# Kernel optimization log

Hardware: AMD Instinct MI355X
Metric: run time of the kernel (lower is better)

The kernel has to match this reference:

```python
import jax, jax.numpy as jnp
import numpy as np

NC = 19
CH16, CH32 = 1024, 2048
B, H, W = 4, 64, 64
EPS = 1e-5


def bn_relu(x, gamma, beta):
    # Train-mode BatchNorm (batch statistics, as in torch default) + ReLU.
    axes = (0,) + tuple(range(2, x.ndim))  # reduce over batch + spatial
    mean = jnp.mean(x, axes, keepdims=True)
    var = jnp.var(x, axes, keepdims=True)
    shp = (1, -1) + (1,) * (x.ndim - 2)
    return jax.nn.relu((x - mean) * jax.lax.rsqrt(var + EPS) * gamma.reshape(shp) + beta.reshape(shp))


def setup_inputs() -> dict:
    key = jax.random.key(0)
    ks = jax.random.split(key, 10)
    def p(k, shape, fan):
        return jax.random.normal(k, shape, jnp.float32) / np.float32(np.sqrt(fan))
    ones = lambda c: jnp.ones((c,), jnp.float32)
    zeros = lambda c: jnp.zeros((c,), jnp.float32)
    return {
        "x": jax.random.normal(ks[0], (B, CH32, H, W), jnp.float32),
        "low_level_feature": jax.random.normal(ks[1], (B, CH16, H, W), jnp.float32),
        "W_L": p(ks[2], (NC, CH16), CH16), "b_L": zeros(NC),
        "W_X": p(ks[3], (512, CH32, 3, 3), CH32 * 9), "g_X": ones(512), "be_X": zeros(512),
        "W_phi": p(ks[4], (256, 512), 512), "g_phi": ones(256), "be_phi": zeros(256),
        "W_psi": p(ks[5], (256, 512), 512), "g_psi": ones(256), "be_psi": zeros(256),
        "W_delta": p(ks[6], (256, 512), 512), "g_delta": ones(256), "be_delta": zeros(256),
        "W_rho": p(ks[7], (512, 256), 256), "g_rho": ones(512), "be_rho": zeros(512),
        "W_g": p(ks[8], (512, 1024), 1024), "g_g": ones(512), "be_g": zeros(512),
        "W_out": p(ks[9], (NC, 512), 512), "b_out": zeros(NC),
    }


def reference(x, low_level_feature, W_L, b_L, W_X, g_X, be_X,
              W_phi, g_phi, be_phi, W_psi, g_psi, be_psi,
              W_delta, g_delta, be_delta, W_rho, g_rho, be_rho,
              W_g, g_g, be_g, W_out, b_out):
    b, _, h, w = x.shape
    # X = conv2d(2048->512, 3x3) + BN + ReLU
    Xf = jax.lax.conv_general_dilated(x, W_X, (1, 1), 'SAME',
                                      dimension_numbers=('NCHW', 'OIHW', 'NCHW'))
    Xf = bn_relu(Xf, g_X, be_X)                          # [b,512,h,w]
    # L = 1x1 conv (with bias) -> soft object regions
    L = jnp.einsum('bchw,nc->bnhw', low_level_feature, W_L) + b_L[None, :, None, None]
    l_flat = L.reshape(b, L.shape[1], -1)                # [b,nc,N]
    M = jax.nn.softmax(l_flat, axis=-1)                  # softmax over N
    X_flat = Xf.reshape(b, 512, -1)                      # [b,512,N]
    # f_k = (M @ X_flat^T)^T : object region features [b,512,nc]
    f_k = jnp.einsum('bkn,bcn->bck', M, X_flat)
    # phi/psi/delta: 1x1 conv1d + BN + ReLU
    query = bn_relu(jnp.einsum('oc,bck->bok', W_phi, f_k), g_phi, be_phi)      # [b,256,nc]
    key_ = bn_relu(jnp.einsum('oc,bcn->bon', W_psi, X_flat), g_psi, be_psi)    # [b,256,N]
    logit = jnp.einsum('bqk,bqn->bkn', query, key_)      # [b,nc,N]
    attn = jax.nn.softmax(logit, axis=1)                 # softmax over nc (dim 1)
    delta = bn_relu(jnp.einsum('oc,bck->bok', W_delta, f_k), g_delta, be_delta)  # [b,256,nc]
    attn_sum = jnp.einsum('bqk,bkn->bqn', delta, attn)   # [b,256,N]
    X_obj = bn_relu(jnp.einsum('oq,bqn->bon', W_rho, attn_sum), g_rho, be_rho)
    X_obj = X_obj.reshape(b, 512, h, w)
    concat = jnp.concatenate([Xf, X_obj], axis=1)        # [b,1024,h,w]
    X_bar = bn_relu(jnp.einsum('oc,bchw->bohw', W_g, concat), g_g, be_g)
    out = jnp.einsum('nc,bchw->bnhw', W_out, X_bar) + b_out[None, :, None, None]
    return out
```

## Files before the change

### kernel.cpp

```cpp
#include <hip/hip_runtime.h>
#include <hip/hip_bf16.h>
#include <cstdint>
#include <cstddef>

#define EPSV 1e-5f

typedef float f32x4 __attribute__((ext_vector_type(4)));
typedef _Float16 f16x8 __attribute__((ext_vector_type(8)));
typedef unsigned short ushortx8 __attribute__((ext_vector_type(8)));

__device__ __forceinline__ unsigned short f2h(float f) {
  _Float16 h = (_Float16)f;
  return *reinterpret_cast<unsigned short*>(&h);
}

__device__ __forceinline__ void gload16(const void* g, void* l) {
  __builtin_amdgcn_global_load_lds(
      (const __attribute__((address_space(1))) void*)g,
      (__attribute__((address_space(3))) void*)l, 16, 0, 0);
}

__global__ __launch_bounds__(256) void ocr_cvt_x(const float* __restrict__ x,
                                                 unsigned short* __restrict__ xT) {
  __shared__ float tile[64][65];
  int icb = blockIdx.x, h = blockIdx.y, b = blockIdx.z, t = threadIdx.x;
  const float* xp = x + ((size_t)b * 2048 + icb * 64) * 4096 + h * 64;
  #pragma unroll
  for (int r = 0; r < 16; ++r) {
    int icl = r * 4 + (t >> 6), w = t & 63;
    tile[icl][w] = xp[(size_t)icl * 4096 + w];
  }
  __syncthreads();
  #pragma unroll
  for (int it = 0; it < 2; ++it) {
    int w = it * 32 + (t >> 3), cb = (t & 7) * 8;
    ushortx8 o;
    #pragma unroll
    for (int j = 0; j < 8; ++j) o[j] = f2h(tile[cb + j][w]);
    *(ushortx8*)&xT[(((size_t)b * 66 + h + 1) * 66 + (w + 1)) * 2048 + icb * 64 + cb] = o;
  }
}

__global__ __launch_bounds__(256) void ocr_cvt_w(const float* __restrict__ Wx,
                                                 unsigned short* __restrict__ WT) {
  int oc = blockIdx.x >> 3;
  int ic = (blockIdx.x & 7) * 256 + threadIdx.x;
  const float* wp = Wx + ((size_t)oc * 2048 + ic) * 9;
  float v[9];
  #pragma unroll
  for (int t = 0; t < 9; ++t) v[t] = wp[t];
  #pragma unroll
  for (int t = 0; t < 9; ++t)
    WT[((size_t)t * 512 + oc) * 2048 + ic] = f2h(v[t]);
}

__global__ __launch_bounds__(256) void ocr_cvt_h2(const float* __restrict__ inA,
                                                  unsigned short* __restrict__ outA,
                                                  const float* __restrict__ inB,
                                                  unsigned short* __restrict__ outB) {
  int i = blockIdx.x * 256 + threadIdx.x;
  if (i < 131072) outA[i] = f2h(inA[i]);
  if (i < 524288) outB[i] = f2h(inB[i]);
}

__global__ __launch_bounds__(1024, 4) void ocr_conv_mfma(const unsigned short* __restrict__ xT,
                                                         const unsigned short* __restrict__ WT,
                                                         float* __restrict__ Xf) {
  __shared__ __align__(16) char lds_raw[163840];
  float* red = (float*)lds_raw;

  const int t = threadIdx.x;
  const int wv = t >> 6, lane = t & 63;
  const int kg = lane >> 4, lc = lane & 15;
  const int ws = wv & 7, kh = wv >> 3;

  const int hg  = blockIdx.x & 7;
  const int b   = (blockIdx.x >> 3) & 3;
  const int oct = blockIdx.x >> 5;
  const int oc0 = oct * 64, h0 = hg * 8;

  const char* gp[5]; int lo[5];
  #pragma unroll
  for (int i = 0; i < 5; ++i) {
    int c = wv * 5 + i;
    lo[i] = c * 1024;
    if (c < 38) {
      int cell = c * 64 + lane; if (cell > 2375) cell = 2375;
      int r = cell / 66, col = cell - r * 66; if (col > 63) col = 63;
      int tap = r >> 2, kgs = r & 3;
      gp[i] = (const char*)WT + (size_t)(((tap * 512 + oc0 + col) * 2048) + kgs * 8) * 2;
    } else {
      int c2 = c - 38;
      int cell = c2 * 64 + lane; if (cell > 2639) cell = 2639;
      int r = cell / 66, col = cell - r * 66;
      int row = r >> 2, kgs = r & 3;
      gp[i] = (const char*)xT + (size_t)((((b * 66 + h0 + row) * 66 + col) * 2048) + kgs * 8) * 2;
    }
  }

  f32x4 acc[4][4] = {};

  #pragma unroll
  for (int i = 0; i < 5; ++i) gload16(gp[i], lds_raw + lo[i]);
  __syncthreads();

  int cur = 0;
  #pragma unroll 1
  for (int step = 0; step < 64; ++step) {
    if (step < 63) {
      unsigned adv = (unsigned)(step + 1) * 64u;
      int nxt = (cur ^ 1) * 81920;
      #pragma unroll
      for (int i = 0; i < 5; ++i) gload16(gp[i] + adv, lds_raw + nxt + lo[i]);
    }
    const short* As = (const short*)(lds_raw + cur * 81920);
    const short* Bs = (const short*)(lds_raw + cur * 81920 + 38912);
    #pragma unroll
    for (int j = 0; j < 5; ++j) {
      const int tap = kh * 4 + j;
      const int dh = tap / 3, dw = tap - dh * 3;
      f16x8 av[4];
      #pragma unroll
      for (int mi = 0; mi < 4; ++mi)
        av[mi] = *(const f16x8*)&As[((tap * 4 + kg) * 66 + mi * 16 + lc) * 8];
      const int row = ws + dh;
      const int nw0 = (tap == 4) ? (kh ? 2 : 0) : 0;
      const int nwN = (tap == 4) ? (nw0 + 2) : 4;
      #pragma unroll
      for (int nw = 0; nw < 4; ++nw) {
        if (nw >= nw0 && nw < nwN) {
          f16x8 bv = *(const f16x8*)&Bs[((row * 4 + kg) * 66 + nw * 16 + lc + dw) * 8];
          #pragma unroll
          for (int mi = 0; mi < 4; ++mi)
            acc[mi][nw] = __builtin_amdgcn_mfma_f32_16x16x32_f16(av[mi], bv, acc[mi][nw], 0, 0, 0);
        }
      }
    }
    __syncthreads();
    cur ^= 1;
  }

  if (kh == 1) {
    #pragma unroll
    for (int mi = 0; mi < 4; ++mi)
      #pragma unroll
      for (int nw = 0; nw < 4; ++nw)
        *(f32x4*)&red[(((ws * 16 + mi * 4 + nw) * 64) + lane) * 4] = acc[mi][nw];
  }
  __syncthreads();
  if (kh == 0) {
    const int h = h0 + ws;
    #pragma unroll
    for (int mi = 0; mi < 4; ++mi) {
      #pragma unroll
      for (int nw = 0; nw < 4; ++nw) {
        f32x4 other = *(const f32x4*)&red[(((ws * 16 + mi * 4 + nw) * 64) + lane) * 4];
        f32x4 s = acc[mi][nw] + other;
        #pragma unroll
        for (int r = 0; r < 4; ++r) {
          int oc = oc0 + mi * 16 + (lane >> 4) * 4 + r;
          int w = nw * 16 + lc;
          Xf[(((size_t)b * 512 + oc) * 64 + h) * 64 + w] = s[r];
        }
      }
    }
  }
}

template<int K, int OT, int NT, int NWM, int NWN, int LDB>
__global__ __launch_bounds__(256) void ocr_gemm_h(const unsigned short* __restrict__ Ah,
                                                  const unsigned short* __restrict__ Bh,
                                                  float* __restrict__ Cm, int O) {
  static_assert(NT == 128, "NT fixed");
  constexpr int MI = OT / NWM / 16;
  constexpr int NI = NT / NWN / 16;
  constexpr int SA = OT + 2, SB = NT + 2;
  constexpr int ACELL = 4 * OT / 256;
  constexpr int ABUF = 4 * SA * 8;
  constexpr int BBUF = 4 * SB * 8;
  constexpr int NS = K / 32;
  constexpr int LPW = ACELL + 2;
  __shared__ __align__(16) short As_s[2 * ABUF];
  __shared__ __align__(16) short Bs_s[2 * BBUF];

  const int t = threadIdx.x;
  const int wv = t >> 6, lane = t & 63;
  const int kg = lane >> 4, lc = lane & 15;
  const int wm = wv / NWN, wn = wv % NWN;

  const int n0 = blockIdx.x * NT, o0 = blockIdx.y * OT, b = blockIdx.z;

  const char* aBase[ACELL]; int aLds[ACELL];
  #pragma unroll
  for (int r = 0; r < ACELL; ++r) {
    int flat0 = r * 256 + (t & 448);
    int flat  = flat0 + lane;
    int kgs = flat / OT, ol = flat % OT;
    aBase[r] = (const char*)(Ah + ((size_t)(o0 + ol)) * K + kgs * 8);
    aLds[r] = ((flat0 / OT) * SA + (flat0 % OT)) * 16;
  }
  const char* bBase[2]; int bLds[2];
  #pragma unroll
  for (int r = 0; r < 2; ++r) {
    int flat0 = r * 256 + (t & 448);
    int flat  = flat0 + lane;
    int kgs = flat >> 7, nl = flat & 127;
    bBase[r] = (const char*)(Bh + ((size_t)b * 4096 + n0 + nl) * LDB + kgs * 8);
    bLds[r] = ((flat0 >> 7) * SB + (flat0 & 127)) * 16;
  }

  f32x4 acc[MI][NI] = {};
  #pragma unroll
  for (int r = 0; r < ACELL; ++r) gload16(aBase[r], (char*)As_s + aLds[r]);
  #pragma unroll
  for (int r = 0; r < 2; ++r) gload16(bBase[r], (char*)Bs_s + bLds[r]);
  asm volatile("s_waitcnt vmcnt(0)" ::: "memory");
  __builtin_amdgcn_s_barrier();

  int cur = 0;
  #pragma unroll 1
  for (int step = 0; step < NS; ++step) {
    if (step + 1 < NS) {
      unsigned adv = (unsigned)(step + 1) * 64u;
      int nA = (cur ^ 1) * ABUF * 2, nB = (cur ^ 1) * BBUF * 2;
      #pragma unroll
      for (int r = 0; r < ACELL; ++r) gload16(aBase[r] + adv, (char*)As_s + nA + aLds[r]);
      #pragma unroll
      for (int r = 0; r < 2; ++r) gload16(bBase[r] + adv, (char*)Bs_s + nB + bLds[r]);
      if constexpr (LPW == 3) asm volatile("s_waitcnt vmcnt(3)" ::: "memory");
      else                    asm volatile("s_waitcnt vmcnt(4)" ::: "memory");
    } else {
      asm volatile("s_waitcnt vmcnt(0)" ::: "memory");
    }
    __builtin_amdgcn_s_barrier();

    const short* As = As_s + cur * ABUF;
    const short* Bsc = Bs_s + cur * BBUF;
    f16x8 av[MI], bv[NI];
    #pragma unroll
    for (int mi = 0; mi < MI; ++mi)
      av[mi] = *(const f16x8*)&As[(kg * SA + wm * (MI * 16) + mi * 16 + lc) * 8];
    #pragma unroll
    for (int ni = 0; ni < NI; ++ni)
      bv[ni] = *(const f16x8*)&Bsc[(kg * SB + wn * (NI * 16) + ni * 16 + lc) * 8];
    __builtin_amdgcn_s_setprio(1);
    #pragma unroll
    for (int mi = 0; mi < MI; ++mi)
      #pragma unroll
      for (int ni = 0; ni < NI; ++ni)
        acc[mi][ni] = __builtin_amdgcn_mfma_f32_16x16x32_f16(av[mi], bv[ni], acc[mi][ni], 0, 0, 0);
    __builtin_amdgcn_s_setprio(0);
    asm volatile("s_waitcnt lgkmcnt(0)" ::: "memory");
    __builtin_amdgcn_sched_barrier(0);
    __builtin_amdgcn_s_barrier();
    cur ^= 1;
  }
  #pragma unroll
  for (int mi = 0; mi < MI; ++mi) {
    #pragma unroll
    for (int ni = 0; ni < NI; ++ni) {
      int n = n0 + wn * (NI * 16) + ni * 16 + lc;
      #pragma unroll
      for (int r = 0; r < 4; ++r) {
        int oc = o0 + wm * (MI * 16) + mi * 16 + (lane >> 4) * 4 + r;
        Cm[((size_t)b * O + oc) * 4096 + n] = acc[mi][ni][r];
      }
    }
  }
}

__global__ __launch_bounds__(256) void ocr_t2h(const float* __restrict__ in,
                                               const float* __restrict__ scale,
                                               const float* __restrict__ shift,
                                               unsigned short* __restrict__ out,
                                               int C, int coff) {
  __shared__ float tile[64][65];
  int n0 = blockIdx.x * 64, c0 = blockIdx.y * 64, b = blockIdx.z;
  int t = threadIdx.x;
  #pragma unroll
  for (int r = 0; r < 16; ++r) {
    int c_l = r * 4 + (t >> 6), n_l = t & 63;
    tile[c_l][n_l] = in[((size_t)(b * C + c0 + c_l)) * 4096 + n0 + n_l];
  }
  __syncthreads();
  int n_l = t >> 2, cb = (t & 3) * 16;
  ushortx8 o0v, o1v;
  #pragma unroll
  for (int j = 0; j < 8; ++j) {
    int c = c0 + cb + j;
    o0v[j] = f2h(fmaxf(0.f, tile[cb + j][n_l] * scale[c] + shift[c]));
  }
  #pragma unroll
  for (int j = 0; j < 8; ++j) {
    int c = c0 + cb + 8 + j;
    o1v[j] = f2h(fmaxf(0.f, tile[cb + 8 + j][n_l] * scale[c] + shift[c]));
  }
  size_t base = ((size_t)b * 4096 + n0 + n_l) * 1024 + coff + c0 + cb;
  *(ushortx8*)&out[base] = o0v;
  *(ushortx8*)&out[base + 8] = o1v;
}

__global__ __launch_bounds__(256) void ocr_chan_stats(const float* __restrict__ buf,
                                                      const float* __restrict__ gamma,
                                                      const float* __restrict__ beta,
                                                      float* __restrict__ scale,
                                                      float* __restrict__ shift, int C) {
  int c = blockIdx.x, t = threadIdx.x;
  float s = 0.f, q = 0.f;
  for (int b = 0; b < 4; ++b) {
    const float* p = buf + ((size_t)b * C + c) * 4096;
    for (int i = t; i < 4096; i += 256) { float v = p[i]; s += v; q += v * v; }
  }
  __shared__ float ls[256], lq[256];
  ls[t] = s; lq[t] = q; __syncthreads();
  for (int off = 128; off > 0; off >>= 1) {
    if (t < off) { ls[t] += ls[t + off]; lq[t] += lq[t + off]; }
    __syncthreads();
  }
  if (t == 0) {
    float mean = ls[0] / 16384.f;
    float var  = lq[0] / 16384.f - mean * mean;
    float sc   = gamma[c] * rsqrtf(var + EPSV);
    scale[c] = sc; shift[c] = beta[c] - mean * sc;
  }
}

__global__ __launch_bounds__(256) void ocr_lproj(const float* __restrict__ llf,
                                                 const float* __restrict__ WL,
                                                 const float* __restrict__ bL,
                                                 float* __restrict__ L) {
  int h = blockIdx.x, b = blockIdx.y;
  int t = threadIdx.x, w = t & 63, csub = t >> 6;
  float acc[19];
  #pragma unroll
  for (int k = 0; k < 19; ++k) acc[k] = 0.f;
  const float* base = llf + ((size_t)b * 1024 + csub * 256) * 4096 + h * 64 + w;
  #pragma unroll 1
  for (int c4 = 0; c4 < 64; ++c4) {
    float lv[4];
    #pragma unroll
    for (int i = 0; i < 4; ++i) lv[i] = base[(size_t)(c4 + i * 64) * 4096];
    #pragma unroll
    for (int i = 0; i < 4; ++i) {
      const float* wl = &WL[csub * 256 + c4 + i * 64];
      #pragma unroll
      for (int k = 0; k < 19; ++k) acc[k] += wl[k * 1024] * lv[i];
    }
  }
  __shared__ float red[4][64][19];
  #pragma unroll
  for (int k = 0; k < 19; ++k) red[csub][w][k] = acc[k];
  __syncthreads();
  if (csub == 0) {
    #pragma unroll
    for (int k = 0; k < 19; ++k) {
      float s = red[0][w][k] + red[1][w][k] + red[2][w][k] + red[3][w][k] + bL[k];
      L[((size_t)b * 19 + k) * 4096 + h * 64 + w] = s;
    }
  }
}

__global__ __launch_bounds__(256) void ocr_softmax4096(float* __restrict__ buf) {
  int row = blockIdx.x, t = threadIdx.x;
  float* p = buf + (size_t)row * 4096;
  __shared__ float ls[256];
  float m = -1e30f;
  for (int i = t; i < 4096; i += 256) m = fmaxf(m, p[i]);
  ls[t] = m; __syncthreads();
  for (int off = 128; off > 0; off >>= 1) { if (t < off) ls[t] = fmaxf(ls[t], ls[t + off]); __syncthreads(); }
  m = ls[0]; __syncthreads();
  float s = 0.f;
  for (int i = t; i < 4096; i += 256) { float e = __expf(p[i] - m); p[i] = e; s += e; }
  ls[t] = s; __syncthreads();
  for (int off = 128; off > 0; off >>= 1) { if (t < off) ls[t] += ls[t + off]; __syncthreads(); }
  float inv = 1.f / ls[0];
  for (int i = t; i < 4096; i += 256) p[i] *= inv;
}

__global__ __launch_bounds__(256) void ocr_fk(const float* __restrict__ M,
                                              const float* __restrict__ Xf,
                                              const float* __restrict__ scale,
                                              const float* __restrict__ shift,
                                              float* __restrict__ fk) {
  int c = blockIdx.x, b = blockIdx.y, t = threadIdx.x;
  float acc[19];
  #pragma unroll
  for (int k = 0; k < 19; ++k) acc[k] = 0.f;
  const float* xp = Xf + ((size_t)b * 512 + c) * 4096;
  const float* mp = M + (size_t)b * 19 * 4096;
  float sc = scale[c], sh = shift[c];
  for (int n = t; n < 4096; n += 256) {
    float xv = fmaxf(0.f, xp[n] * sc + sh);
    #pragma unroll
    for (int k = 0; k < 19; ++k) acc[k] += mp[k * 4096 + n] * xv;
  }
  __shared__ float red[19 * 256];
  #pragma unroll
  for (int k = 0; k < 19; ++k) red[k * 256 + t] = acc[k];
  __syncthreads();
  for (int off = 128; off > 0; off >>= 1) {
    if (t < off) {
      #pragma unroll
      for (int k = 0; k < 19; ++k) red[k * 256 + t] += red[k * 256 + t + off];
    }
    __syncthreads();
  }
  if (t < 19) fk[((size_t)b * 512 + c) * 19 + t] = red[t * 256];
}

__global__ __launch_bounds__(256) void ocr_qd2(const float* __restrict__ Wphi,
                                               const float* __restrict__ Wdelta,
                                               const float* __restrict__ fk,
                                               float* __restrict__ qry,
                                               float* __restrict__ dlt) {
  int blk = blockIdx.x;
  const float* Wm = (blk < 76) ? Wphi : Wdelta;
  float* out = (blk < 76) ? qry : dlt;
  int tid = (blk < 76 ? blk : blk - 76) * 256 + threadIdx.x;
  if (tid >= 4 * 256 * 19) return;
  int k = tid % 19, o = (tid / 19) % 256, b = tid / (19 * 256);
  const float* fp = fk + (size_t)b * 512 * 19 + k;
  const float* wp = Wm + (size_t)o * 512;
  float acc = 0.f;
  for (int c = 0; c < 512; ++c) acc += wp[c] * fp[c * 19];
  out[tid] = acc;
}

__global__ __launch_bounds__(128) void ocr_bn76x2(float* __restrict__ qry,
                                                  float* __restrict__ dlt,
                                                  const float* __restrict__ g_phi,
                                                  const float* __restrict__ be_phi,
                                                  const float* __restrict__ g_delta,
                                                  const float* __restrict__ be_delta) {
  bool second = blockIdx.x >= 256;
  int o = blockIdx.x & 255, t = threadIdx.x;
  float* buf = second ? dlt : qry;
  const float* gamma = second ? g_delta : g_phi;
  const float* beta  = second ? be_delta : be_phi;
  bool act = t < 76;
  float v = 0.f;
  size_t idx = 0;
  if (act) {
    int b = t / 19, k = t % 19;
    idx = ((size_t)b * 256 + o) * 19 + k;
    v = buf[idx];
  }
  __shared__ float ls[128], lq[128];
  ls[t] = act ? v : 0.f; lq[t] = act ? v * v : 0.f; __syncthreads();
  for (int off = 64; off > 0; off >>= 1) { if (t < off) { ls[t] += ls[t + off]; lq[t] += lq[t + off]; } __syncthreads(); }
  __shared__ float s_sc, s_sh;
  if (t == 0) {
    float mean = ls[0] / 76.f;
    float var  = lq[0] / 76.f - mean * mean;
    float sc   = gamma[o] * rsqrtf(var + EPSV);
    s_sc = sc; s_sh = beta[o] - mean * sc;
  }
  __syncthreads();
  if (act) buf[idx] = fmaxf(0.f, v * s_sc + s_sh);
}

__global__ __launch_bounds__(256) void ocr_attn(const float* __restrict__ query,
                                                const float* __restrict__ key,
                                                const float* __restrict__ scale,
                                                const float* __restrict__ shift,
                                                float* __restrict__ attn) {
  int n0 = blockIdx.x * 64, b = blockIdx.y;
  int t = threadIdx.x, nl = t & 63, qsub = t >> 6;
  __shared__ float ql[256 * 19];
  for (int i = t; i < 256 * 19; i += 256) ql[i] = query[(size_t)b * 256 * 19 + i];
  __syncthreads();
  float acc[19];
  #pragma unroll
  for (int k = 0; k < 19; ++k) acc[k] = 0.f;
  const float* kp = key + ((size_t)b * 256 + qsub * 64) * 4096 + n0 + nl;
  #pragma unroll 1
  for (int q4 = 0; q4 < 64; q4 += 4) {
    float kv[4];
    #pragma unroll
    for (int i = 0; i < 4; ++i) kv[i] = kp[(size_t)(q4 + i) * 4096];
    #pragma unroll
    for (int i = 0; i < 4; ++i) {
      int ch = qsub * 64 + q4 + i;
      float kva = fmaxf(0.f, kv[i] * scale[ch] + shift[ch]);
      const float* qq = &ql[ch * 19];
      #pragma unroll
      for (int k = 0; k < 19; ++k) acc[k] += qq[k] * kva;
    }
  }
  __shared__ float red[4][64][19];
  #pragma unroll
  for (int k = 0; k < 19; ++k) red[qsub][nl][k] = acc[k];
  __syncthreads();
  if (qsub == 0) {
    float v[19]; float m = -1e30f;
    #pragma unroll
    for (int k = 0; k < 19; ++k) {
      v[k] = red[0][nl][k] + red[1][nl][k] + red[2][nl][k] + red[3][nl][k];
      m = fmaxf(m, v[k]);
    }
    float s = 0.f;
    #pragma unroll
    for (int k = 0; k < 19; ++k) { v[k] = __expf(v[k] - m); s += v[k]; }
    float inv = 1.f / s;
    #pragma unroll
    for (int k = 0; k < 19; ++k)
      attn[((size_t)b * 19 + k) * 4096 + n0 + nl] = v[k] * inv;
  }
}

__global__ __launch_bounds__(256) void ocr_wd(const float* __restrict__ Wrho,
                                              const float* __restrict__ dlt,
                                              float* __restrict__ Wd) {
  int tid = blockIdx.x * 256 + threadIdx.x;
  if (tid >= 4 * 512 * 19) return;
  int k = tid % 19, o = (tid / 19) % 512, b = tid / (19 * 512);
  const float* dp = dlt + (size_t)b * 256 * 19 + k;
  const float* wp = Wrho + (size_t)o * 256;
  float acc = 0.f;
  for (int q = 0; q < 256; ++q) acc += wp[q] * dp[q * 19];
  Wd[tid] = acc;
}

__global__ __launch_bounds__(256) void ocr_xobj_stats(const float* __restrict__ Wd,
                                                      const float* __restrict__ attn,
                                                      const float* __restrict__ gamma,
                                                      const float* __restrict__ beta,
                                                      float* __restrict__ scale,
                                                      float* __restrict__ shift) {
  int o = blockIdx.x, t = threadIdx.x;
  float s = 0.f, q = 0.f;
  for (int b = 0; b < 4; ++b) {
    float wd[19];
    #pragma unroll
    for (int k = 0; k < 19; ++k) wd[k] = Wd[((size_t)b * 512 + o) * 19 + k];
    for (int n = t; n < 4096; n += 256) {
      float v = 0.f;
      #pragma unroll
      for (int k = 0; k < 19; ++k) v += wd[k] * attn[((size_t)b * 19 + k) * 4096 + n];
      s += v; q += v * v;
    }
  }
  __shared__ float ls[256], lq[256];
  ls[t] = s; lq[t] = q; __syncthreads();
  for (int off = 128; off > 0; off >>= 1) {
    if (t < off) { ls[t] += ls[t + off]; lq[t] += lq[t + off]; }
    __syncthreads();
  }
  if (t == 0) {
    float mean = ls[0] / 16384.f;
    float var  = lq[0] / 16384.f - mean * mean;
    float sc   = gamma[o] * rsqrtf(var + EPSV);
    scale[o] = sc; shift[o] = beta[o] - mean * sc;
  }
}

__global__ __launch_bounds__(512) void ocr_xobj_apply(const float* __restrict__ Wd,
                                                      const float* __restrict__ attn,
                                                      const float* __restrict__ scale,
                                                      const float* __restrict__ shift,
                                                      unsigned short* __restrict__ ch) {
  __shared__ float al[19][256];
  int n0 = blockIdx.x * 256, b = blockIdx.y, o = threadIdx.x;
  for (int idx = o; idx < 19 * 256; idx += 512) {
    int k = idx >> 8, nl = idx & 255;
    al[k][nl] = attn[((size_t)b * 19 + k) * 4096 + n0 + nl];
  }
  float wd[19];
  #pragma unroll
  for (int k = 0; k < 19; ++k) wd[k] = Wd[((size_t)b * 512 + o) * 19 + k];
  float sc = scale[o], sh = shift[o];
  __syncthreads();
  #pragma unroll 1
  for (int nl = 0; nl < 256; ++nl) {
    float v = 0.f;
    #pragma unroll
    for (int k = 0; k < 19; ++k) v += wd[k] * al[k][nl];
    v = fmaxf(0.f, v * sc + sh);
    ch[((size_t)b * 4096 + n0 + nl) * 1024 + 512 + o] = f2h(v);
  }
}

__global__ __launch_bounds__(256) void ocr_out(const float* __restrict__ Wout,
                                               const float* __restrict__ bout,
                                               const float* __restrict__ Xbar,
                                               const float* __restrict__ scale,
                                               const float* __restrict__ shift,
                                               float* __restrict__ out) {
  int n0 = blockIdx.x * 64, b = blockIdx.y;
  int t = threadIdx.x, nl = t & 63, csub = t >> 6;
  float acc[19];
  #pragma unroll
  for (int k = 0; k < 19; ++k) acc[k] = 0.f;
  const float* base = Xbar + ((size_t)b * 512 + csub * 128) * 4096 + n0 + nl;
  #pragma unroll 1
  for (int c4 = 0; c4 < 128; c4 += 4) {
    float xv[4];
    #pragma unroll
    for (int i = 0; i < 4; ++i) xv[i] = base[(size_t)(c4 + i) * 4096];
    #pragma unroll
    for (int i = 0; i < 4; ++i) {
      int chn = csub * 128 + c4 + i;
      float a = fmaxf(0.f, xv[i] * scale[chn] + shift[chn]);
      #pragma unroll
      for (int k = 0; k < 19; ++k) acc[k] += Wout[k * 512 + chn] * a;
    }
  }
  __shared__ float red[4][64][19];
  #pragma unroll
  for (int k = 0; k < 19; ++k) red[csub][nl][k] = acc[k];
  __syncthreads();
  if (csub == 0) {
    #pragma unroll
    for (int k = 0; k < 19; ++k) {
      float s = red[0][nl][k] + red[1][nl][k] + red[2][nl][k] + red[3][nl][k] + bout[k];
      out[((size_t)b * 19 + k) * 4096 + n0 + nl] = s;
    }
  }
}

extern "C" void kernel_launch(void* const* d_in, const int* in_sizes, int n_in,
                              void* d_out, int out_size, void* d_ws, size_t ws_size,
                              hipStream_t stream) {
  const float* x    = (const float*)d_in[0];
  const float* llf  = (const float*)d_in[1];
  const float* W_L  = (const float*)d_in[2];
  const float* b_L  = (const float*)d_in[3];
  const float* W_X  = (const float*)d_in[4];
  const float* g_X  = (const float*)d_in[5];
  const float* be_X = (const float*)d_in[6];
  const float* W_phi = (const float*)d_in[7];
  const float* g_phi = (const float*)d_in[8];
  const float* be_phi = (const float*)d_in[9];
  const float* W_psi = (const float*)d_in[10];
  const float* g_psi = (const float*)d_in[11];
  const float* be_psi = (const float*)d_in[12];
  const float* W_delta = (const float*)d_in[13];
  const float* g_delta = (const float*)d_in[14];
  const float* be_delta = (const float*)d_in[15];
  const float* W_rho = (const float*)d_in[16];
  const float* g_rho = (const float*)d_in[17];
  const float* be_rho = (const float*)d_in[18];
  const float* W_g  = (const float*)d_in[19];
  const float* g_g  = (const float*)d_in[20];
  const float* be_g = (const float*)d_in[21];
  const float* W_out = (const float*)d_in[22];
  const float* b_out = (const float*)d_in[23];

  float* ws = (float*)d_ws;
  float* Xf = ws;
  float* U  = ws + 8388608;
  unsigned short* xT = (unsigned short*)U;
  unsigned short* WT = (unsigned short*)(U + 17842176);
  unsigned short* concat_h = (unsigned short*)U;
  float* key  = U + 8388608;
  float* Xbar = U + 12582912;
  float* SM   = U + 22560768;
  float* M     = SM;
  float* attnb = SM + 311296;
  float* fk    = SM + 622592;
  float* qry   = SM + 661504;
  float* dlt   = SM + 680960;
  float* Wd    = SM + 700416;
  float* st    = SM + 739328;
  unsigned short* Wpsi_h = (unsigned short*)(SM + 743424);
  unsigned short* Wg_h   = (unsigned short*)(SM + 808960);
  float* scX = st,        *shX = st + 512;
  float* scP = st + 1024, *shP = st + 1280;
  float* scR = st + 1536, *shR = st + 2048;
  float* scG = st + 2560, *shG = st + 3072;

  hipMemsetAsync(xT, 0, (size_t)35684352 * sizeof(unsigned short), stream);
  ocr_cvt_x<<<dim3(32, 64, 4), 256, 0, stream>>>(x, xT);
  ocr_cvt_w<<<dim3(4096), 256, 0, stream>>>(W_X, WT);
  ocr_cvt_h2<<<dim3(2048), 256, 0, stream>>>(W_psi, Wpsi_h, W_g, Wg_h);

  ocr_conv_mfma<<<dim3(256), 1024, 0, stream>>>(xT, WT, Xf);

  ocr_chan_stats<<<dim3(512), 256, 0, stream>>>(Xf, g_X, be_X, scX, shX, 512);
  ocr_t2h<<<dim3(64, 8, 4), 256, 0, stream>>>(Xf, scX, shX, concat_h, 512, 0);
  ocr_lproj<<<dim3(64, 4), 256, 0, stream>>>(llf, W_L, b_L, M);
  ocr_softmax4096<<<dim3(76), 256, 0, stream>>>(M);
  ocr_fk<<<dim3(512, 4), 256, 0, stream>>>(M, Xf, scX, shX, fk);
  ocr_qd2<<<dim3(152), 256, 0, stream>>>(W_phi, W_delta, fk, qry, dlt);
  ocr_bn76x2<<<dim3(512), 128, 0, stream>>>(qry, dlt, g_phi, be_phi, g_delta, be_delta);
  ocr_gemm_h<512, 64, 128, 2, 2, 1024><<<dim3(32, 4, 4), 256, 0, stream>>>(Wpsi_h, concat_h, key, 256);
  ocr_chan_stats<<<dim3(256), 256, 0, stream>>>(key, g_psi, be_psi, scP, shP, 256);
  ocr_attn<<<dim3(64, 4), 256, 0, stream>>>(qry, key, scP, shP, attnb);
  ocr_wd<<<dim3(152), 256, 0, stream>>>(W_rho, dlt, Wd);
  ocr_xobj_stats<<<dim3(512), 256, 0, stream>>>(Wd, attnb, g_rho, be_rho, scR, shR);
  ocr_xobj_apply<<<dim3(16, 4), 512, 0, stream>>>(Wd, attnb, scR, shR, concat_h);
  ocr_gemm_h<1024, 128, 128, 2, 2, 1024><<<dim3(32, 4, 4), 256, 0, stream>>>(Wg_h, concat_h, Xbar, 512);
  ocr_chan_stats<<<dim3(512), 256, 0, stream>>>(Xbar, g_g, be_g, scG, shG, 512);
  ocr_out<<<dim3(64, 4), 256, 0, stream>>>(W_out, b_out, Xbar, scG, shG, (float*)d_out);
}
```

Baseline: 748.6 us.

## Shrink conv blocks, zero only halo, compute X_obj BN stats via Gram

Replaces the full memset of the padded transposed input with a kernel that zeroes only the halo rows and columns. Restructures the conv kernel into 512-thread blocks covering 4 output rows each, with a single-buffered 64KB LDS stage instead of double buffering, so more blocks fit per CU. It also computes the X_obj BatchNorm statistics algebraically from a 19x19 Gram matrix of the attention maps plus row sums, rather than materialising every projected value. The conv change gives up load/compute overlap and adds barriers per step, and the Gram path relies on float atomics, which makes summation order nondeterministic.

```diff
diff --git a/kernel.cpp b/kernel.cpp
--- a/kernel.cpp
+++ b/kernel.cpp
@@ -18,6 +18,22 @@
   __builtin_amdgcn_global_load_lds(
       (const __attribute__((address_space(1))) void*)g,
       (__attribute__((address_space(3))) void*)l, 16, 0, 0);
+}
+
+__global__ __launch_bounds__(256) void ocr_halo_zero(unsigned short* __restrict__ xT) {
+  int e = blockIdx.x, b = blockIdx.y, t = threadIdx.x;
+  ushortx8 z = {0, 0, 0, 0, 0, 0, 0, 0};
+  if (e < 2) {
+    int row = e ? 65 : 0;
+    ushortx8* p = (ushortx8*)(xT + (size_t)(b * 66 + row) * 66 * 2048);
+    for (int i = t; i < 66 * 256; i += 256) p[i] = z;
+  } else {
+    int col = (e == 3) ? 65 : 0;
+    for (int idx = t; idx < 64 * 256; idx += 256) {
+      int r = (idx >> 8) + 1, v = idx & 255;
+      ((ushortx8*)(xT + ((size_t)(b * 66 + r) * 66 + col) * 2048))[v] = z;
+    }
+  }
 }
 
 __global__ __launch_bounds__(256) void ocr_cvt_x(const float* __restrict__ x,
@@ -63,58 +79,55 @@
   if (i < 524288) outB[i] = f2h(inB[i]);
 }
 
-__global__ __launch_bounds__(1024, 4) void ocr_conv_mfma(const unsigned short* __restrict__ xT,
-                                                         const unsigned short* __restrict__ WT,
-                                                         float* __restrict__ Xf) {
-  __shared__ __align__(16) char lds_raw[163840];
+__global__ __launch_bounds__(512, 4) void ocr_conv_mfma(const unsigned short* __restrict__ xT,
+                                                        const unsigned short* __restrict__ WT,
+                                                        float* __restrict__ Xf) {
+  __shared__ __align__(16) char lds_raw[65536];
   float* red = (float*)lds_raw;
 
   const int t = threadIdx.x;
   const int wv = t >> 6, lane = t & 63;
   const int kg = lane >> 4, lc = lane & 15;
-  const int ws = wv & 7, kh = wv >> 3;
-
-  const int hg  = blockIdx.x & 7;
-  const int b   = (blockIdx.x >> 3) & 3;
-  const int oct = blockIdx.x >> 5;
-  const int oc0 = oct * 64, h0 = hg * 8;
-
-  const char* gp[5]; int lo[5];
-  #pragma unroll
-  for (int i = 0; i < 5; ++i) {
-    int c = wv * 5 + i;
-    lo[i] = c * 1024;
-    if (c < 38) {
-      int cell = c * 64 + lane; if (cell > 2375) cell = 2375;
+  const int ws = wv & 3, kh = wv >> 2;
+
+  const int bx = blockIdx.x;
+  const int hg  = ((bx & 7) << 1) | ((bx >> 3) & 1);
+  const int b   = (bx >> 4) & 3;
+  const int oct = bx >> 6;
+  const int oc0 = oct * 64, h0 = hg * 4;
+
+  const char* gp[8]; int lo[8]; bool go[8];
+  #pragma unroll
+  for (int i = 0; i < 8; ++i) {
+    int c = wv * 8 + i;
+    go[i] = c < 63;
+    int cc = go[i] ? c : 0;
+    if (cc < 38) {
+      int cell = cc * 64 + lane; if (cell > 2375) cell = 2375;
       int r = cell / 66, col = cell - r * 66; if (col > 63) col = 63;
       int tap = r >> 2, kgs = r & 3;
       gp[i] = (const char*)WT + (size_t)(((tap * 512 + oc0 + col) * 2048) + kgs * 8) * 2;
+      lo[i] = cc * 1024;
     } else {
-      int c2 = c - 38;
-      int cell = c2 * 64 + lane; if (cell > 2639) cell = 2639;
+      int c2 = cc - 38;
+      int cell = c2 * 64 + lane; if (cell > 1583) cell = 1583;
       int r = cell / 66, col = cell - r * 66;
       int row = r >> 2, kgs = r & 3;
       gp[i] = (const char*)xT + (size_t)((((b * 66 + h0 + row) * 66 + col) * 2048) + kgs * 8) * 2;
+      lo[i] = 38912 + c2 * 1024;
     }
   }
 
   f32x4 acc[4][4] = {};
 
   #pragma unroll
-  for (int i = 0; i < 5; ++i) gload16(gp[i], lds_raw + lo[i]);
-  __syncthreads();
-
-  int cur = 0;
+  for (int i = 0; i < 8; ++i) if (go[i]) gload16(gp[i], lds_raw + lo[i]);
+  __syncthreads();
+
   #pragma unroll 1
   for (int step = 0; step < 64; ++step) {
-    if (step < 63) {
-      unsigned adv = (unsigned)(step + 1) * 64u;
-      int nxt = (cur ^ 1) * 81920;
-      #pragma unroll
-      for (int i = 0; i < 5; ++i) gload16(gp[i] + adv, lds_raw + nxt + lo[i]);
-    }
-    const short* As = (const short*)(lds_raw + cur * 81920);
-    const short* Bs = (const short*)(lds_raw + cur * 81920 + 38912);
+    const short* As = (const short*)lds_raw;
+    const short* Bs = (const short*)(lds_raw + 38912);
     #pragma unroll
     for (int j = 0; j < 5; ++j) {
       const int tap = kh * 4 + j;
@@ -136,10 +149,16 @@
         }
       }
     }
-    __syncthreads();
-    cur ^= 1;
-  }
-
+    if (step < 63) {
+      __syncthreads();
+      unsigned adv = (unsigned)(step + 1) * 64u;
+      #pragma unroll
+      for (int i = 0; i < 8; ++i) if (go[i]) gload16(gp[i] + adv, lds_raw + lo[i]);
+      __syncthreads();
+    }
+  }
+
+  __syncthreads();
   if (kh == 1) {
     #pragma unroll
     for (int mi = 0; mi < 4; ++mi)
@@ -521,37 +540,57 @@
   Wd[tid] = acc;
 }
 
-__global__ __launch_bounds__(256) void ocr_xobj_stats(const float* __restrict__ Wd,
-                                                      const float* __restrict__ attn,
-                                                      const float* __restrict__ gamma,
-                                                      const float* __restrict__ beta,
-                                                      float* __restrict__ scale,
-                                                      float* __restrict__ shift) {
-  int o = blockIdx.x, t = threadIdx.x;
+__global__ __launch_bounds__(384) void ocr_gram(const float* __restrict__ attn,
+                                                float* __restrict__ G,
+                                                float* __restrict__ RS) {
+  __shared__ float al[19][513];
+  int n0 = blockIdx.x * 512, b = blockIdx.y, t = threadIdx.x;
+  for (int i = t; i < 19 * 512; i += 384) {
+    int k = i >> 9, n = i & 511;
+    al[k][n] = attn[((size_t)b * 19 + k) * 4096 + n0 + n];
+  }
+  __syncthreads();
+  if (t < 361) {
+    int k1 = t / 19, k2 = t % 19;
+    float s = 0.f;
+    for (int n = 0; n < 512; ++n) s += al[k1][n] * al[k2][n];
+    atomicAdd(&G[(b * 19 + k1) * 19 + k2], s);
+  } else if (t < 380) {
+    int k = t - 361;
+    float s = 0.f;
+    for (int n = 0; n < 512; ++n) s += al[k][n];
+    atomicAdd(&RS[b * 19 + k], s);
+  }
+}
+
+__global__ __launch_bounds__(512) void ocr_xobj_fin(const float* __restrict__ Wd,
+                                                    const float* __restrict__ G,
+                                                    const float* __restrict__ RS,
+                                                    const float* __restrict__ gamma,
+                                                    const float* __restrict__ beta,
+                                                    float* __restrict__ scale,
+                                                    float* __restrict__ shift) {
+  int o = threadIdx.x;
   float s = 0.f, q = 0.f;
   for (int b = 0; b < 4; ++b) {
     float wd[19];
     #pragma unroll
     for (int k = 0; k < 19; ++k) wd[k] = Wd[((size_t)b * 512 + o) * 19 + k];
-    for (int n = t; n < 4096; n += 256) {
-      float v = 0.f;
-      #pragma unroll
-      for (int k = 0; k < 19; ++k) v += wd[k] * attn[((size_t)b * 19 + k) * 4096 + n];
-      s += v; q += v * v;
-    }
-  }
-  __shared__ float ls[256], lq[256];
-  ls[t] = s; lq[t] = q; __syncthreads();
-  for (int off = 128; off > 0; off >>= 1) {
-    if (t < off) { ls[t] += ls[t + off]; lq[t] += lq[t + off]; }
-    __syncthreads();
-  }
-  if (t == 0) {
-    float mean = ls[0] / 16384.f;
-    float var  = lq[0] / 16384.f - mean * mean;
-    float sc   = gamma[o] * rsqrtf(var + EPSV);
-    scale[o] = sc; shift[o] = beta[o] - mean * sc;
-  }
+    const float* g = &G[b * 361];
+    const float* rs = &RS[b * 19];
+    #pragma unroll
+    for (int k = 0; k < 19; ++k) s += wd[k] * rs[k];
+    for (int k1 = 0; k1 < 19; ++k1) {
+      float tacc = 0.f;
+      #pragma unroll
+      for (int k2 = 0; k2 < 19; ++k2) tacc += g[k1 * 19 + k2] * wd[k2];
+      q += wd[k1] * tacc;
+    }
+  }
+  float mean = s / 16384.f;
+  float var  = q / 16384.f - mean * mean;
+  float sc   = gamma[o] * rsqrtf(var + EPSV);
+  scale[o] = sc; shift[o] = beta[o] - mean * sc;
 }
 
 __global__ __launch_bounds__(512) void ocr_xobj_apply(const float* __restrict__ Wd,
@@ -664,17 +703,20 @@
   float* st    = SM + 739328;
   unsigned short* Wpsi_h = (unsigned short*)(SM + 743424);
   unsigned short* Wg_h   = (unsigned short*)(SM + 808960);
+  float* Gm    = SM + 1071104;
+  float* RSm   = SM + 1072548;
   float* scX = st,        *shX = st + 512;
   float* scP = st + 1024, *shP = st + 1280;
   float* scR = st + 1536, *shR = st + 2048;
   float* scG = st + 2560, *shG = st + 3072;
 
-  hipMemsetAsync(xT, 0, (size_t)35684352 * sizeof(unsigned short), stream);
+  ocr_halo_zero<<<dim3(4, 4), 256, 0, stream>>>(xT);
   ocr_cvt_x<<<dim3(32, 64, 4), 256, 0, stream>>>(x, xT);
   ocr_cvt_w<<<dim3(4096), 256, 0, stream>>>(W_X, WT);
   ocr_cvt_h2<<<dim3(2048), 256, 0, stream>>>(W_psi, Wpsi_h, W_g, Wg_h);
-
-  ocr_conv_mfma<<<dim3(256), 1024, 0, stream>>>(xT, WT, Xf);
+  hipMemsetAsync(Gm, 0, 1520 * sizeof(float), stream);
+
+  ocr_conv_mfma<<<dim3(512), 512, 0, stream>>>(xT, WT, Xf);
 
   ocr_chan_stats<<<dim3(512), 256, 0, stream>>>(Xf, g_X, be_X, scX, shX, 512);
   ocr_t2h<<<dim3(64, 8, 4), 256, 0, stream>>>(Xf, scX, shX, concat_h, 512, 0);
@@ -687,7 +729,8 @@
   ocr_chan_stats<<<dim3(256), 256, 0, stream>>>(key, g_psi, be_psi, scP, shP, 256);
   ocr_attn<<<dim3(64, 4), 256, 0, stream>>>(qry, key, scP, shP, attnb);
   ocr_wd<<<dim3(152), 256, 0, stream>>>(W_rho, dlt, Wd);
-  ocr_xobj_stats<<<dim3(512), 256, 0, stream>>>(Wd, attnb, g_rho, be_rho, scR, shR);
+  ocr_gram<<<dim3(8, 4), 384, 0, stream>>>(attnb, Gm, RSm);
+  ocr_xobj_fin<<<dim3(1), 512, 0, stream>>>(Wd, Gm, RSm, g_rho, be_rho, scR, shR);
   ocr_xobj_apply<<<dim3(16, 4), 512, 0, stream>>>(Wd, attnb, scR, shR, concat_h);
   ocr_gemm_h<1024, 128, 128, 2, 2, 1024><<<dim3(32, 4, 4), 256, 0, stream>>>(Wg_h, concat_h, Xbar, 512);
   ocr_chan_stats<<<dim3(512), 256, 0, stream>>>(Xbar, g_g, be_g, scG, shG, 512);
```

Result: slower. 815.3 us (+8.9%).
